# Kernel tuning notes

Measured on AMD Instinct MI355X. Metric: run time of the kernel, lower is better.

## Reference

```python
import jax, jax.numpy as jnp
import numpy as np
import math

B, A, IN_C, OUT_C = 64, 128, 128, 64

def _l2norm(x, eps=1e-12):
    # matches F.normalize(dim=1) on 2D input: x / max(||x||_2, eps) along last dim
    n = jnp.sqrt(jnp.sum(x * x, axis=-1, keepdims=True))
    return x / jnp.maximum(n, eps)

def setup_inputs() -> dict:
    key = jax.random.key(0)
    ks = jax.random.split(key, 7)
    s = 1.0 / math.sqrt(IN_C)
    return {
        "features": jax.random.normal(ks[0], (B, IN_C, A), dtype=jnp.float32),
        "Wq": jax.random.uniform(ks[1], (OUT_C, IN_C), jnp.float32, -s, s),
        "bq": jax.random.uniform(ks[2], (OUT_C,), jnp.float32, -s, s),
        "Wk": jax.random.uniform(ks[3], (OUT_C, IN_C), jnp.float32, -s, s),
        "bk": jax.random.uniform(ks[4], (OUT_C,), jnp.float32, -s, s),
        "Wv": jax.random.uniform(ks[5], (OUT_C, IN_C), jnp.float32, -s, s),
        "bv": jax.random.uniform(ks[6], (OUT_C,), jnp.float32, -s, s),
    }

def reference(features, Wq, bq, Wk, bk, Wv, bv):
    b = features.shape[0]
    f = jnp.transpose(features, (0, 2, 1))          # (b, a, in_c)
    a = f.shape[1]
    q = f @ Wq.T + bq                               # (b, a, d)
    k = f @ Wk.T + bk
    v = f @ Wv.T + bv
    d = q.shape[-1]
    qf = q.reshape(-1, d)                           # (N, d), N = b*a
    kf = k.reshape(-1, d)
    vf = v.reshape(-1, d)
    att = jax.nn.softmax(qf @ kf.T / math.sqrt(d), axis=1)  # (N, N)
    qkv = att @ vf                                  # (N, d)
    qkv_n = _l2norm(qkv).reshape(b, a, d)
    v_n = _l2norm(vf).reshape(b, a, d)
    # sim_s[i,j] = (1/a) * sum_t v_n[i,t] . qkv_n[j,t]  (diagonal-trace over 'a')
    sim_s = jnp.einsum('bad,cad->bc', v_n, qkv_n) / a
    return sim_s
```

## Files before the change

kernel.cpp:

```cpp
#include <hip/hip_runtime.h>
#include <hip/hip_bf16.h>

#define NROW 8192
#define INC  128
#define OUTC 64
#define BG   16

#define QSCALE 0.18033688011112042f

typedef __bf16 bf16x8 __attribute__((ext_vector_type(8)));
typedef __bf16 bf16x4 __attribute__((ext_vector_type(4)));
typedef short  s16x4  __attribute__((ext_vector_type(4)));
typedef short  s16x8  __attribute__((ext_vector_type(8)));
typedef float  f32x4  __attribute__((ext_vector_type(4)));

static __device__ __forceinline__ f32x4 mfma16(bf16x8 a, bf16x8 b, f32x4 c) {
    return __builtin_amdgcn_mfma_f32_16x16x32_bf16(a, b, c, 0, 0, 0);
}
static __device__ __forceinline__ f32x4 mfma1k(s16x4 a, s16x4 b, f32x4 c) {
    return __builtin_amdgcn_mfma_f32_16x16x16bf16_1k(a, b, c, 0, 0, 0);
}

static __device__ __forceinline__ bf16x8 cvt8(float4 lo, float4 hi) {
    bf16x8 r;
    r[0] = (__bf16)lo.x; r[1] = (__bf16)lo.y; r[2] = (__bf16)lo.z; r[3] = (__bf16)lo.w;
    r[4] = (__bf16)hi.x; r[5] = (__bf16)hi.y; r[6] = (__bf16)hi.z; r[7] = (__bf16)hi.w;
    return r;
}
static __device__ __forceinline__ s16x4 vlo(s16x8 x) {
    return __builtin_shufflevector(x, x, 0, 1, 2, 3);
}
static __device__ __forceinline__ s16x4 vhi(s16x8 x) {
    return __builtin_shufflevector(x, x, 4, 5, 6, 7);
}

__global__ __launch_bounds__(256) void proj_kernel(
    const float* __restrict__ feat,
    const float* __restrict__ Wq, const float* __restrict__ bq,
    const float* __restrict__ Wk, const float* __restrict__ bk,
    const float* __restrict__ Wv, const float* __restrict__ bv,
    __hip_bfloat16* __restrict__ qbf, __hip_bfloat16* __restrict__ kbf,
    __hip_bfloat16* __restrict__ vbf, __hip_bfloat16* __restrict__ vnb)
{
    __shared__ float slab[32 * 132];
    __shared__ float vbuf[32 * 66];
    __shared__ float invb[32];

    const int tid = threadIdx.x;
    const int w    = tid >> 6;
    const int lane = tid & 63;
    const int l16  = lane & 15;
    const int quad = lane >> 4;

    const int b   = blockIdx.x >> 2;
    const int a0  = (blockIdx.x & 3) * 32;
    const int r0  = b * 128 + a0;
    const float* fb = feat + (size_t)b * INC * 128;

    for (int i = tid; i < 32 * 128; i += 256) {
        int c = i >> 5, a = i & 31;
        slab[a * 132 + c] = fb[c * 128 + a0 + a];
    }
    __syncthreads();

    f32x4 acc[3][2];
    #pragma unroll
    for (int t = 0; t < 3; ++t)
        #pragma unroll
        for (int u = 0; u < 2; ++u)
            acc[t][u] = (f32x4){0.f, 0.f, 0.f, 0.f};

    #pragma unroll
    for (int kc = 0; kc < 4; ++kc) {
        const int k0 = kc * 32 + quad * 8;
        bf16x8 afr[2];
        #pragma unroll
        for (int u = 0; u < 2; ++u) {
            const float* ar = slab + (u * 16 + l16) * 132 + k0;
            afr[u] = cvt8(*(const float4*)ar, *(const float4*)(ar + 4));
        }
        #pragma unroll
        for (int t = 0; t < 3; ++t) {
            const int tile = w * 3 + t;
            const int mat  = tile >> 2;
            const float* W = (mat == 0) ? Wq : (mat == 1) ? Wk : Wv;
            const float* wr = W + ((tile & 3) * 16 + l16) * INC + k0;
            bf16x8 bfr = cvt8(*(const float4*)wr, *(const float4*)(wr + 4));
            #pragma unroll
            for (int u = 0; u < 2; ++u)
                acc[t][u] = mfma16(afr[u], bfr, acc[t][u]);
        }
    }

    #pragma unroll
    for (int t = 0; t < 3; ++t) {
        const int tile = w * 3 + t;
        const int mat  = tile >> 2;
        const int nt   = tile & 3;
        const float* bias = (mat == 0) ? bq : (mat == 1) ? bk : bv;
        const float bl = bias[nt * 16 + l16];
        if (mat == 0) {
            #pragma unroll
            for (int u = 0; u < 2; ++u) {
                const int base = ((((r0 >> 4) + u) * 4 + nt) << 8) + l16;
                #pragma unroll
                for (int r = 0; r < 4; ++r)
                    qbf[base + (quad * 4 + r) * 16] =
                        __float2bfloat16((acc[t][u][r] + bl) * QSCALE);
            }
        } else if (mat == 1) {
            const int kq = (r0 >> 5) * 2048 + (nt >> 1) * 512 +
                           ((nt & 1) * 2 + (l16 >> 3)) * 128 + quad * 32 + (l16 & 7);
            #pragma unroll
            for (int u = 0; u < 2; ++u)
                #pragma unroll
                for (int r = 0; r < 4; ++r)
                    kbf[kq + u * 1024 + r * 8] = __float2bfloat16(acc[t][u][r] + bl);
        } else {
            #pragma unroll
            for (int u = 0; u < 2; ++u)
                #pragma unroll
                for (int r = 0; r < 4; ++r)
                    vbuf[(u * 16 + quad * 4 + r) * 66 + nt * 16 + l16] = acc[t][u][r] + bl;
        }
    }
    __syncthreads();

    const int rl = tid >> 3;
    const int jj = tid & 7;
    float ss = 0.f;
    #pragma unroll
    for (int i = 0; i < 8; ++i) {
        float x = vbuf[rl * 66 + jj * 8 + i];
        ss += x * x;
    }
    ss += __shfl_xor(ss, 1, 64);
    ss += __shfl_xor(ss, 2, 64);
    ss += __shfl_xor(ss, 4, 64);
    if (jj == 0) invb[rl] = rsqrtf(fmaxf(ss, 1e-24f));
    __syncthreads();
    float inv = invb[rl];
    bf16x8 vpk;
    #pragma unroll
    for (int i = 0; i < 8; ++i)
        vpk[i] = (__bf16)(vbuf[rl * 66 + jj * 8 + i] * inv);
    *(bf16x8*)(vnb + (size_t)(r0 + rl) * 64 + jj * 8) = vpk;

    const int tl = tid & 15;
    const int n  = (tid >> 4) & 3;
    const int s_ = tid >> 6;
    bf16x8 pack;
    #pragma unroll
    for (int j = 0; j < 8; ++j) {
        int key = s_ * 8 + j;
        pack[j] = (__bf16)(vbuf[key * 66 + n * 16 + tl] * invb[key]);
    }
    const int e1 = (r0 >> 5) * 2048 + (s_ >> 1) * 1024 + (n >> 1) * 512 +
                   (s_ & 1) * 256 + tl * 8 + (n & 1) * 4;
    bf16x4 plo = __builtin_shufflevector(pack, pack, 0, 1, 2, 3);
    bf16x4 phi = __builtin_shufflevector(pack, pack, 4, 5, 6, 7);
    *(bf16x4*)(vbf + e1)       = plo;
    *(bf16x4*)(vbf + e1 + 128) = phi;
}

#define STAGE_W(BUF, KR, VR) do {                                            \
        *(float4*)((BUF) + stb) = KR;                                        \
        *(float4*)((BUF) + 4096 + stb) = VR; } while (0)
#define STAGE_L(KR, VR) do {                                                 \
        KR = *(const float4*)gk; VR = *(const float4*)gv;                    \
        gk += 4096; gv += 4096; } while (0)

#define BARRIER_KEEP_VMCNT() do {                                            \
        asm volatile("s_waitcnt lgkmcnt(0)" ::: "memory");                   \
        __builtin_amdgcn_s_barrier(); } while (0)

#define COMPUTE(BUF) do {                                                    \
    const char* kbp = (BUF);                                                 \
    const char* vbp = (BUF) + 4096;                                          \
    bf16x8 k00 = *(const bf16x8*)(kbp + lb);                                 \
    bf16x8 k01 = *(const bf16x8*)(kbp + lb + 1024);                          \
    bf16x8 k10 = *(const bf16x8*)(kbp + lb + 2048);                          \
    bf16x8 k11 = *(const bf16x8*)(kbp + lb + 3072);                          \
    s16x8 W0 = *(const s16x8*)(vbp + lb);                                    \
    s16x8 W1 = *(const s16x8*)(vbp + lb + 1024);                             \
    s16x8 W2 = *(const s16x8*)(vbp + lb + 2048);                             \
    s16x8 W3 = *(const s16x8*)(vbp + lb + 3072);                             \
    const f32x4 zero = (f32x4){0.f, 0.f, 0.f, 0.f};                          \
    _Pragma("unroll")                                                        \
    for (int u = 0; u < 4; ++u) {                                            \
        f32x4 s0 = mfma16(k00, qf32[u][0], zero);                            \
        s0       = mfma16(k01, qf32[u][1], s0);                              \
        f32x4 s1 = mfma16(k10, qf32[u][0], zero);                            \
        s1       = mfma16(k11, qf32[u][1], s1);                              \
        union { bf16x4 v; s16x4 s; } pf0, pf1;                               \
        _Pragma("unroll")                                                    \
        for (int r = 0; r < 4; ++r) {                                        \
            float p0 = __builtin_amdgcn_exp2f(s0[r]);                        \
            float p1 = __builtin_amdgcn_exp2f(s1[r]);                        \
            lp[u] += p0 + p1;                                                \
            pf0.v[r] = (__bf16)p0;                                           \
            pf1.v[r] = (__bf16)p1;                                           \
        }                                                                    \
        of[u][0] = mfma1k(pf0.s, vlo(W0), of[u][0]);                         \
        of[u][0] = mfma1k(pf1.s, vlo(W2), of[u][0]);                         \
        of[u][1] = mfma1k(pf0.s, vhi(W0), of[u][1]);                         \
        of[u][1] = mfma1k(pf1.s, vhi(W2), of[u][1]);                         \
        of[u][2] = mfma1k(pf0.s, vlo(W1), of[u][2]);                         \
        of[u][2] = mfma1k(pf1.s, vlo(W3), of[u][2]);                         \
        of[u][3] = mfma1k(pf0.s, vhi(W1), of[u][3]);                         \
        of[u][3] = mfma1k(pf1.s, vhi(W3), of[u][3]);                         \
    } } while (0)

__global__ __launch_bounds__(256, 2) void attn_kernel(
    const __hip_bfloat16* __restrict__ qbf,
    const __hip_bfloat16* __restrict__ kbf,
    const __hip_bfloat16* __restrict__ vbf,
    float* __restrict__ Opart, float* __restrict__ lpart,
    float* __restrict__ outz)
{
    __shared__ __align__(16) char pool[16384];
    char* bufA = pool;
    char* bufB = pool + 8192;

    const int tid = threadIdx.x;
    if (blockIdx.x == 0) {
        #pragma unroll
        for (int z = 0; z < 4; ++z)
            ((float4*)outz)[tid * 4 + z] = (float4){0.f, 0.f, 0.f, 0.f};
    }

    const int w    = tid >> 6;
    const int lane = tid & 63;
    const int l16  = lane & 15;
    const int quad = lane >> 4;
    const int qb   = blockIdx.x >> 4;
    const int bg   = blockIdx.x & 15;
    const int r0   = qb * 256 + w * 64;
    const int fo32 = l16 * 16 + (quad & 1) * 8;
    const int qh   = quad >> 1;
    const int lb   = lane * 16;
    const int stb  = tid * 16;

    bf16x8 qf32[4][2];
    #pragma unroll
    for (int u = 0; u < 4; ++u)
        #pragma unroll
        for (int p = 0; p < 2; ++p)
            qf32[u][p] = *(const bf16x8*)(qbf +
                ((((r0 >> 4) + u) * 4 + p * 2 + qh) << 8) + fo32);

    f32x4 of[4][4];
    float lp[4] = {0.f, 0.f, 0.f, 0.f};
    #pragma unroll
    for (int u = 0; u < 4; ++u)
        #pragma unroll
        for (int n = 0; n < 4; ++n)
            of[u][n] = (f32x4){0.f, 0.f, 0.f, 0.f};

    const char* gk = (const char*)kbf + (size_t)(bg * 16) * 4096 + stb;
    const char* gv = (const char*)vbf + (size_t)(bg * 16) * 4096 + stb;

    float4 ka, va, kb_, vb_;
    STAGE_L(ka, va);
    STAGE_W(bufA, ka, va);
    STAGE_L(kb_, vb_);
    BARRIER_KEEP_VMCNT();

    #pragma unroll 1
    for (int body = 0; body < 7; ++body) {
        STAGE_W(bufB, kb_, vb_);
        STAGE_L(ka, va);
        COMPUTE(bufA);
        BARRIER_KEEP_VMCNT();
        STAGE_W(bufA, ka, va);
        STAGE_L(kb_, vb_);
        COMPUTE(bufB);
        BARRIER_KEEP_VMCNT();
    }
    STAGE_W(bufB, kb_, vb_);
    COMPUTE(bufA);
    BARRIER_KEEP_VMCNT();
    COMPUTE(bufB);

    #pragma unroll
    for (int u = 0; u < 4; ++u) {
        float v = lp[u];
        v += __shfl_xor(v, 16, 64);
        v += __shfl_xor(v, 32, 64);
        lp[u] = v;
    }

    #pragma unroll
    for (int u = 0; u < 4; ++u)
        #pragma unroll
        for (int n = 0; n < 4; ++n)
            #pragma unroll
            for (int r = 0; r < 4; ++r)
                Opart[((size_t)(r0 + u * 16 + quad * 4 + r) * 16 + bg) * 64
                      + n * 16 + l16] = of[u][n][r];
    if (quad == 0) {
        #pragma unroll
        for (int u = 0; u < 4; ++u)
            lpart[(r0 + u * 16 + l16) * 16 + bg] = lp[u];
    }
}

__global__ __launch_bounds__(512) void finish_kernel(
    const float* __restrict__ Opart, const float* __restrict__ lpart,
    const __hip_bfloat16* __restrict__ vnb,
    float* __restrict__ out)
{
    __shared__ __hip_bfloat16 qn[64][68];

    const int a   = blockIdx.x;
    const int tid = threadIdx.x;

    {
        const int b  = tid >> 3;
        const int c8 = tid & 7;
        const int r  = b * 128 + a;
        float acc[8] = {0.f, 0.f, 0.f, 0.f, 0.f, 0.f, 0.f, 0.f};
        #pragma unroll
        for (int g = 0; g < 16; ++g) {
            const float* src = Opart + ((size_t)r * 16 + g) * 64 + c8 * 8;
            float4 t0 = *(const float4*)(src);
            float4 t1 = *(const float4*)(src + 4);
            acc[0] += t0.x; acc[1] += t0.y; acc[2] += t0.z; acc[3] += t0.w;
            acc[4] += t1.x; acc[5] += t1.y; acc[6] += t1.z; acc[7] += t1.w;
        }
        float lsum = lpart[r * 16 + c8 * 2] + lpart[r * 16 + c8 * 2 + 1];
        lsum += __shfl_xor(lsum, 1, 64);
        lsum += __shfl_xor(lsum, 2, 64);
        lsum += __shfl_xor(lsum, 4, 64);
        const float inv_l = 1.0f / lsum;
        float ss = 0.f;
        #pragma unroll
        for (int c = 0; c < 8; ++c) {
            acc[c] *= inv_l;
            ss += acc[c] * acc[c];
        }
        ss += __shfl_xor(ss, 1, 64);
        ss += __shfl_xor(ss, 2, 64);
        ss += __shfl_xor(ss, 4, 64);
        const float inv = rsqrtf(fmaxf(ss, 1e-24f));
        bf16x8 pk;
        #pragma unroll
        for (int c = 0; c < 8; ++c)
            pk[c] = (__bf16)(acc[c] * inv);
        *(bf16x8*)&qn[b][c8 * 8] = pk;
    }
    __syncthreads();

    {
        const int w    = tid >> 6;
        const int lane = tid & 63;
        const int l16  = lane & 15;
        const int quad = lane >> 4;
        const int ks   = w & 1;
        const int mi   = w >> 1;
        const int dq   = ks * 32 + quad * 8;

        bf16x8 af = *(const bf16x8*)(vnb +
            (size_t)(mi * 16 + l16) * 8192 + a * 64 + dq);
        f32x4 accd[4];
        #pragma unroll
        for (int ni = 0; ni < 4; ++ni) {
            bf16x8 bfv = *(const bf16x8*)&qn[ni * 16 + l16][dq];
            accd[ni] = mfma16(af, bfv, (f32x4){0.f, 0.f, 0.f, 0.f});
        }
        #pragma unroll
        for (int ni = 0; ni < 4; ++ni)
            #pragma unroll
            for (int r = 0; r < 4; ++r)
                atomicAdd(&out[(mi * 16 + quad * 4 + r) * 64 + ni * 16 + l16],
                          accd[ni][r] * (1.f / 128.f));
    }
}

extern "C" void kernel_launch(void* const* d_in, const int* in_sizes, int n_in,
                              void* d_out, int out_size, void* d_ws, size_t ws_size,
                              hipStream_t stream)
{
    const float* feat = (const float*)d_in[0];
    const float* Wq   = (const float*)d_in[1];
    const float* bq   = (const float*)d_in[2];
    const float* Wk   = (const float*)d_in[3];
    const float* bk   = (const float*)d_in[4];
    const float* Wv   = (const float*)d_in[5];
    const float* bv   = (const float*)d_in[6];
    float* out = (float*)d_out;

    const size_t MB = 1u << 20;
    char* ws = (char*)d_ws;
    __hip_bfloat16* qbf = (__hip_bfloat16*)(ws);
    __hip_bfloat16* kbf = (__hip_bfloat16*)(ws + 1 * MB);
    __hip_bfloat16* vbf = (__hip_bfloat16*)(ws + 2 * MB);
    __hip_bfloat16* vnb = (__hip_bfloat16*)(ws + 3 * MB);
    float* Opart = (float*)(ws + 4 * MB);
    float* lpart = (float*)(ws + 36 * MB);

    proj_kernel<<<256, 256, 0, stream>>>(feat, Wq, bq, Wk, bk, Wv, bv,
                                         qbf, kbf, vbf, vnb);
    attn_kernel<<<512, 256, 0, stream>>>(qbf, kbf, vbf, Opart, lpart, out);
    finish_kernel<<<128, 512, 0, stream>>>(Opart, lpart, vnb, out);
}
```

Baseline: 113.2 us.

## Drop softmax denominator since L2 normalization cancels row scaling; split finish kernel

The attention kernel no longer accumulates the softmax row sums, because the following per-row L2 normalization of qkv makes any positive per-row scale irrelevant. This removes an add per exponential in the inner loop, the cross-lane reductions, and the lpart stores and loads. The finish kernel is also split into two blocks per position, each handling half of the output columns, with 256 threads and a smaller shared tile. The cost is that the eps clamp now applies to unnormalized magnitudes, which only matters for near-zero rows.

```diff
diff --git a/kernel.cpp b/kernel.cpp
--- a/kernel.cpp
+++ b/kernel.cpp
@@ -195,11 +195,8 @@
         union { bf16x4 v; s16x4 s; } pf0, pf1;                               \
         _Pragma("unroll")                                                    \
         for (int r = 0; r < 4; ++r) {                                        \
-            float p0 = __builtin_amdgcn_exp2f(s0[r]);                        \
-            float p1 = __builtin_amdgcn_exp2f(s1[r]);                        \
-            lp[u] += p0 + p1;                                                \
-            pf0.v[r] = (__bf16)p0;                                           \
-            pf1.v[r] = (__bf16)p1;                                           \
+            pf0.v[r] = (__bf16)__builtin_amdgcn_exp2f(s0[r]);                \
+            pf1.v[r] = (__bf16)__builtin_amdgcn_exp2f(s1[r]);                \
         }                                                                    \
         of[u][0] = mfma1k(pf0.s, vlo(W0), of[u][0]);                         \
         of[u][0] = mfma1k(pf1.s, vlo(W2), of[u][0]);                         \
@@ -215,7 +212,7 @@
     const __hip_bfloat16* __restrict__ qbf,
     const __hip_bfloat16* __restrict__ kbf,
     const __hip_bfloat16* __restrict__ vbf,
-    float* __restrict__ Opart, float* __restrict__ lpart,
+    float* __restrict__ Opart,
     float* __restrict__ outz)
 {
     __shared__ __align__(16) char pool[16384];
@@ -250,7 +247,6 @@
                 ((((r0 >> 4) + u) * 4 + p * 2 + qh) << 8) + fo32);
 
     f32x4 of[4][4];
-    float lp[4] = {0.f, 0.f, 0.f, 0.f};
     #pragma unroll
     for (int u = 0; u < 4; ++u)
         #pragma unroll
@@ -283,14 +279,6 @@
     COMPUTE(bufB);
 
     #pragma unroll
-    for (int u = 0; u < 4; ++u) {
-        float v = lp[u];
-        v += __shfl_xor(v, 16, 64);
-        v += __shfl_xor(v, 32, 64);
-        lp[u] = v;
-    }
-
-    #pragma unroll
     for (int u = 0; u < 4; ++u)
         #pragma unroll
         for (int n = 0; n < 4; ++n)
@@ -298,27 +286,23 @@
             for (int r = 0; r < 4; ++r)
                 Opart[((size_t)(r0 + u * 16 + quad * 4 + r) * 16 + bg) * 64
                       + n * 16 + l16] = of[u][n][r];
-    if (quad == 0) {
-        #pragma unroll
-        for (int u = 0; u < 4; ++u)
-            lpart[(r0 + u * 16 + l16) * 16 + bg] = lp[u];
-    }
-}
-
-__global__ __launch_bounds__(512) void finish_kernel(
-    const float* __restrict__ Opart, const float* __restrict__ lpart,
+}
+
+__global__ __launch_bounds__(256) void finish_kernel(
+    const float* __restrict__ Opart,
     const __hip_bfloat16* __restrict__ vnb,
     float* __restrict__ out)
 {
-    __shared__ __hip_bfloat16 qn[64][68];
-
-    const int a   = blockIdx.x;
-    const int tid = threadIdx.x;
+    __shared__ __hip_bfloat16 qn[32][68];
+
+    const int a     = blockIdx.x >> 1;
+    const int jhalf = blockIdx.x & 1;
+    const int tid   = threadIdx.x;
 
     {
-        const int b  = tid >> 3;
+        const int bl = tid >> 3;
         const int c8 = tid & 7;
-        const int r  = b * 128 + a;
+        const int r  = (jhalf * 32 + bl) * 128 + a;
         float acc[8] = {0.f, 0.f, 0.f, 0.f, 0.f, 0.f, 0.f, 0.f};
         #pragma unroll
         for (int g = 0; g < 16; ++g) {
@@ -328,17 +312,10 @@
             acc[0] += t0.x; acc[1] += t0.y; acc[2] += t0.z; acc[3] += t0.w;
             acc[4] += t1.x; acc[5] += t1.y; acc[6] += t1.z; acc[7] += t1.w;
         }
-        float lsum = lpart[r * 16 + c8 * 2] + lpart[r * 16 + c8 * 2 + 1];
-        lsum += __shfl_xor(lsum, 1, 64);
-        lsum += __shfl_xor(lsum, 2, 64);
-        lsum += __shfl_xor(lsum, 4, 64);
-        const float inv_l = 1.0f / lsum;
         float ss = 0.f;
         #pragma unroll
-        for (int c = 0; c < 8; ++c) {
-            acc[c] *= inv_l;
+        for (int c = 0; c < 8; ++c)
             ss += acc[c] * acc[c];
-        }
         ss += __shfl_xor(ss, 1, 64);
         ss += __shfl_xor(ss, 2, 64);
         ss += __shfl_xor(ss, 4, 64);
@@ -347,7 +324,7 @@
         #pragma unroll
         for (int c = 0; c < 8; ++c)
             pk[c] = (__bf16)(acc[c] * inv);
-        *(bf16x8*)&qn[b][c8 * 8] = pk;
+        *(bf16x8*)&qn[bl][c8 * 8] = pk;
     }
     __syncthreads();
 
@@ -356,23 +333,27 @@
         const int lane = tid & 63;
         const int l16  = lane & 15;
         const int quad = lane >> 4;
-        const int ks   = w & 1;
-        const int mi   = w >> 1;
-        const int dq   = ks * 32 + quad * 8;
-
-        bf16x8 af = *(const bf16x8*)(vnb +
-            (size_t)(mi * 16 + l16) * 8192 + a * 64 + dq);
-        f32x4 accd[4];
-        #pragma unroll
-        for (int ni = 0; ni < 4; ++ni) {
-            bf16x8 bfv = *(const bf16x8*)&qn[ni * 16 + l16][dq];
-            accd[ni] = mfma16(af, bfv, (f32x4){0.f, 0.f, 0.f, 0.f});
-        }
-        #pragma unroll
-        for (int ni = 0; ni < 4; ++ni)
+
+        f32x4 accd[2];
+        accd[0] = (f32x4){0.f, 0.f, 0.f, 0.f};
+        accd[1] = (f32x4){0.f, 0.f, 0.f, 0.f};
+        #pragma unroll
+        for (int ks = 0; ks < 2; ++ks) {
+            const int dq = ks * 32 + quad * 8;
+            bf16x8 af = *(const bf16x8*)(vnb +
+                (size_t)(w * 16 + l16) * 8192 + a * 64 + dq);
+            #pragma unroll
+            for (int ni = 0; ni < 2; ++ni) {
+                bf16x8 bfv = *(const bf16x8*)&qn[ni * 16 + l16][dq];
+                accd[ni] = mfma16(af, bfv, accd[ni]);
+            }
+        }
+        #pragma unroll
+        for (int ni = 0; ni < 2; ++ni)
             #pragma unroll
             for (int r = 0; r < 4; ++r)
-                atomicAdd(&out[(mi * 16 + quad * 4 + r) * 64 + ni * 16 + l16],
+                atomicAdd(&out[(w * 16 + quad * 4 + r) * 64 +
+                               jhalf * 32 + ni * 16 + l16],
                           accd[ni][r] * (1.f / 128.f));
     }
 }
@@ -397,10 +378,9 @@
     __hip_bfloat16* vbf = (__hip_bfloat16*)(ws + 2 * MB);
     __hip_bfloat16* vnb = (__hip_bfloat16*)(ws + 3 * MB);
     float* Opart = (float*)(ws + 4 * MB);
-    float* lpart = (float*)(ws + 36 * MB);
 
     proj_kernel<<<256, 256, 0, stream>>>(feat, Wq, bq, Wk, bk, Wv, bv,
                                          qbf, kbf, vbf, vnb);
-    attn_kernel<<<512, 256, 0, stream>>>(qbf, kbf, vbf, Opart, lpart, out);
-    finish_kernel<<<128, 512, 0, stream>>>(Opart, lpart, vnb, out);
-}
+    attn_kernel<<<512, 256, 0, stream>>>(qbf, kbf, vbf, Opart, out);
+    finish_kernel<<<256, 256, 0, stream>>>(Opart, vnb, out);
+}
```

Result: faster. 110.3 us (-2.5%).
